# Kernel tuning notes

Measured on AMD Instinct MI355X. Metric: run time of the kernel, lower is better.

The kernel has to match this reference:

```python
import jax, jax.numpy as jnp
import numpy as np

D_MODEL = 64
N_HEADS = 4
D_K = 16
D_FF = 512
N_LAYERS = 6
SRC_V = 83
DEG_V = 21
DIST_V = 200
B, L = 256, 128


def _positional_encoding(length, d_model):
    pos = np.arange(length, dtype=np.float32)[:, None]
    div = np.exp(np.arange(0, d_model, 2, dtype=np.float32) * (-np.log(10000.0) / d_model))
    pe = np.zeros((length, d_model), dtype=np.float32)
    pe[:, 0::2] = np.sin(pos * div)
    pe[:, 1::2] = np.cos(pos * div)
    return jnp.asarray(pe)


def _layernorm(x, eps=1e-5):
    mu = jnp.mean(x, axis=-1, keepdims=True)
    var = jnp.mean((x - mu) ** 2, axis=-1, keepdims=True)
    return (x - mu) / jnp.sqrt(var + eps)


def setup_inputs() -> dict:
    key = jax.random.key(0)
    ks = jax.random.split(key, 12)
    s = 0.02
    enc_inputs = jax.random.randint(ks[0], (B, L), 0, SRC_V)
    degree_s = jax.random.randint(ks[1], (B, L), 0, DEG_V)
    MD = jax.random.randint(ks[2], (B, L, L), 0, DIST_V)
    src_emb = (jax.random.normal(ks[3], (SRC_V, D_MODEL)) * s).at[0].set(0.0)   # padding_idx=0
    deg_emb = (jax.random.normal(ks[4], (DEG_V, D_MODEL)) * s).at[20].set(0.0)  # padding_idx=20
    md_emb = (jax.random.normal(ks[5], (DIST_V, N_HEADS)) * s).at[0].set(0.0)   # padding_idx=0
    Wq = jax.random.normal(ks[6], (N_LAYERS, D_MODEL, N_HEADS * D_K)) * s
    Wk = jax.random.normal(ks[7], (N_LAYERS, D_MODEL, N_HEADS * D_K)) * s
    Wv = jax.random.normal(ks[8], (N_LAYERS, D_MODEL, N_HEADS * D_K)) * s
    Wo = jax.random.normal(ks[9], (N_LAYERS, N_HEADS * D_K, D_MODEL)) * s
    W1 = jax.random.normal(ks[10], (N_LAYERS, D_MODEL, D_FF)) * s
    W2 = jax.random.normal(ks[11], (N_LAYERS, D_FF, D_MODEL)) * s
    return dict(enc_inputs=enc_inputs, degree_s=degree_s, MD=MD,
                src_emb=src_emb, deg_emb=deg_emb, md_emb=md_emb,
                Wq=Wq, Wk=Wk, Wv=Wv, Wo=Wo, W1=W1, W2=W2)


def reference(enc_inputs, degree_s, MD, src_emb, deg_emb, md_emb, Wq, Wk, Wv, Wo, W1, W2):
    b, l = enc_inputs.shape
    x = src_emb[enc_inputs] + deg_emb[degree_s] + _positional_encoding(l, D_MODEL)[None]
    # pad mask: key token == 0 -> masked; broadcast [B,1,1,L] over heads & queries
    pad_mask = (enc_inputs == 0)[:, None, None, :]
    # distance bias: [B,L,L,H] -> [B,H,L,L]
    bias = jnp.transpose(md_emb[MD], (0, 3, 1, 2))
    scale = 1.0 / np.sqrt(D_K).astype(np.float32)
    for i in range(N_LAYERS):
        q = (x @ Wq[i]).reshape(b, l, N_HEADS, D_K).transpose(0, 2, 1, 3)
        k = (x @ Wk[i]).reshape(b, l, N_HEADS, D_K).transpose(0, 2, 1, 3)
        v = (x @ Wv[i]).reshape(b, l, N_HEADS, D_K).transpose(0, 2, 1, 3)
        scores = jnp.einsum('bhqd,bhkd->bhqk', q, k) * scale + bias
        scores = jnp.where(pad_mask, -1e9, scores)
        attn = jax.nn.softmax(scores, axis=-1)
        ctx = jnp.einsum('bhqk,bhkd->bhqd', attn, v).transpose(0, 2, 1, 3).reshape(b, l, N_HEADS * D_K)
        x = _layernorm(ctx @ Wo[i] + x)
        x = _layernorm(jax.nn.relu(x @ W1[i]) @ W2[i] + x)
    return x
```

## Files before the change

kernel.cpp:

```cpp
#include <hip/hip_runtime.h>
#include <hip/hip_bf16.h>
#include <stdint.h>

#define DI __device__ __forceinline__

namespace {

constexpr int BB  = 256;
constexpr int LL  = 128;
constexpr int DM  = 64;
constexpr int DFF = 512;
constexpr int NL  = 6;
constexpr int TT  = BB * LL;

typedef __attribute__((ext_vector_type(8))) short bf16x8;
typedef __attribute__((ext_vector_type(4))) float f32x4;

DI float bf2f(uint16_t u) { union { uint32_t i; float f; } w; w.i = (uint32_t)u << 16; return w.f; }
DI uint16_t f2bf(float f) {
  union { float f; uint32_t i; } w; w.f = f;
  uint32_t r = (w.i + 0x7fffu + ((w.i >> 16) & 1u)) >> 16;
  return (uint16_t)r;
}
DI uint32_t pack2(float a, float b) { return (uint32_t)f2bf(a) | ((uint32_t)f2bf(b) << 16); }

DI bf16x8 fragld(const uint16_t* __restrict__ base, int ld, int lane) {
  return *(const bf16x8*)(base + (size_t)(lane & 15) * ld + (lane >> 4) * 8);
}
DI f32x4 MFMA(bf16x8 a, bf16x8 b, f32x4 c) {
  return __builtin_amdgcn_mfma_f32_16x16x32_bf16(a, b, c, 0, 0, 0);
}

__global__ void __launch_bounds__(256) k_embed(const int* __restrict__ enc, const int* __restrict__ deg,
    const float* __restrict__ semb, const float* __restrict__ demb,
    float* __restrict__ x, uint16_t* __restrict__ xb) {
  int idx = blockIdx.x * 256 + threadIdx.x;
  int t = idx >> 6, d = idx & 63;
  int l = t & (LL - 1);
  float e = (float)(d & ~1) * -0.14391156831212787f;
  float ang = (float)l * __expf(e);
  float pe = (d & 1) ? __cosf(ang) : __sinf(ang);
  float v = semb[enc[t] * DM + d] + demb[deg[t] * DM + d] + pe;
  x[idx] = v;
  xb[idx] = f2bf(v);
}

__global__ void __launch_bounds__(256) k_trans(const float* __restrict__ w, uint16_t* __restrict__ wt,
    int K, int O, int dstStride, int colOff) {
  int idx = blockIdx.x * 256 + threadIdx.x;
  int KO = K * O;
  int mat = idx / KO;
  int rem = idx - mat * KO;
  int c = rem / K;
  int k = rem - c * K;
  wt[(size_t)mat * dstStride + (size_t)(colOff + c) * K + k] = f2bf(w[((size_t)mat * K + k) * O + c]);
}

__global__ void __launch_bounds__(256) k_bias2(const int* __restrict__ MD, const float* __restrict__ memb,
    const int* __restrict__ enc, uint16_t* __restrict__ biasT) {
  int o = blockIdx.x * 256 + threadIdx.x;
  int b  = o >> 14;
  int r  = (o >> 7) & (LL - 1);
  int kk = o & (LL - 1);
  bool mask = (enc[b * LL + kk] == 0);
  int md = MD[o];
  float4 m = *(const float4*)(memb + md * 4);
  float mv[4] = {m.x, m.y, m.z, m.w};
#pragma unroll
  for (int h = 0; h < 4; ++h) {
    uint16_t v = mask ? (uint16_t)0xce6eu : f2bf(mv[h]);
    biasT[(((size_t)(b * 4 + h) * LL) + r) * LL + kk] = v;
  }
}

DI void ln_write(float (&v)[4][4], float (&xfh)[4][4], uint16_t* __restrict__ xls,
                 int r0, int g, int c) {
  float sum[4], sq[4];
#pragma unroll
  for (int j = 0; j < 4; ++j) sum[j] = (v[j][0] + v[j][1]) + (v[j][2] + v[j][3]);
#pragma unroll
  for (int off = 1; off < 16; off <<= 1)
#pragma unroll
    for (int j = 0; j < 4; ++j) sum[j] += __shfl_xor(sum[j], off, 64);
#pragma unroll
  for (int j = 0; j < 4; ++j) {
    float mu = sum[j] * 0.015625f;
#pragma unroll
    for (int ct = 0; ct < 4; ++ct) v[j][ct] -= mu;
    sq[j] = (v[j][0] * v[j][0] + v[j][1] * v[j][1]) + (v[j][2] * v[j][2] + v[j][3] * v[j][3]);
  }
#pragma unroll
  for (int off = 1; off < 16; off <<= 1)
#pragma unroll
    for (int j = 0; j < 4; ++j) sq[j] += __shfl_xor(sq[j], off, 64);
#pragma unroll
  for (int j = 0; j < 4; ++j) {
    float rstd = rsqrtf(sq[j] * 0.015625f + 1e-5f);
#pragma unroll
    for (int ct = 0; ct < 4; ++ct) {
      float r = v[j][ct] * rstd;
      xfh[ct][j] = r;
      xls[(r0 + g * 4 + j) * 72 + ct * 16 + c] = f2bf(r);
    }
  }
}

__global__ void __launch_bounds__(512, 1) k_mega(
    const float* __restrict__ x0, const uint16_t* __restrict__ xb0,
    const uint16_t* __restrict__ biasT,
    const uint16_t* __restrict__ wtqkv, const uint16_t* __restrict__ wto,
    const uint16_t* __restrict__ wt1, const uint16_t* __restrict__ wt2,
    float* __restrict__ out) {
  __shared__ __align__(16) char LDSB[119808];
  int tid = threadIdx.x;
  int w8 = tid >> 6, lane = tid & 63;
  int g = lane >> 4, c = lane & 15;
  int h = w8 & 3, half = w8 >> 2;
  int b = blockIdx.x;

  uint16_t* xls  = (uint16_t*)(LDSB);
  uint16_t* klsA = (uint16_t*)(LDSB + 18432);
  uint16_t* klsh = (uint16_t*)(LDSB + 18432 + h * 10240);
  uint16_t* vtlh = (uint16_t*)(LDSB + 59392 + h * 4352);
  uint16_t* qsc  = (uint16_t*)(LDSB + 76800 + w8 * 1280);
  char*     ptl  = LDSB + 87040 + w8 * 4096;
  uint16_t* ctxl = (uint16_t*)(LDSB + 18432);
  uint16_t* hidl = (uint16_t*)(LDSB + 36864 + w8 * 8448);

  float xf[4][4];
  const float* xrow = x0 + ((size_t)b * LL + w8 * 16) * DM;
#pragma unroll
  for (int ct = 0; ct < 4; ++ct)
#pragma unroll
    for (int j = 0; j < 4; ++j)
      xf[ct][j] = xrow[(g * 4 + j) * DM + ct * 16 + c];
  const uint16_t* xbrow = xb0 + (size_t)b * LL * DM;
#pragma unroll
  for (int m = 0; m < 2; ++m) {
    int u = tid * 2 + m;
    int r = u >> 3, col = (u & 7) * 8;
    *(bf16x8*)(xls + r * 72 + col) = *(const bf16x8*)(xbrow + r * DM + col);
  }
  __syncthreads();

  for (int li = 0; li < NL; ++li) {
#pragma unroll
    for (int m = 0; m < 2; ++m) {
      int idx = tid * 2 + m;
      int head = idx >> 8, r = (idx >> 1) & 127, s = idx & 1;
      *(uint4*)(klsA + head * 5120 + r * 40 + 16 + s * 8) = uint4{0, 0, 0, 0};
    }
    if (lane < 32) {
      int r = lane >> 1, s = lane & 1;
      *(uint4*)(qsc + r * 40 + 16 + s * 8) = uint4{0, 0, 0, 0};
    }

    const uint16_t* Wl = wtqkv + (size_t)li * 192 * 64;
    bf16x8 bq0 = fragld(Wl + (h * 16) * 64, 64, lane);
    bf16x8 bq1 = fragld(Wl + (h * 16) * 64 + 32, 64, lane);
    bf16x8 bk0 = fragld(Wl + (64 + h * 16) * 64, 64, lane);
    bf16x8 bk1 = fragld(Wl + (64 + h * 16) * 64 + 32, 64, lane);
    bf16x8 bv0 = fragld(Wl + (128 + h * 16) * 64, 64, lane);
    bf16x8 bv1 = fragld(Wl + (128 + h * 16) * 64 + 32, 64, lane);
    uint2 qreg[4];
#pragma unroll
    for (int rt = 0; rt < 4; ++rt) {
      int r0 = half * 64 + rt * 16;
      bf16x8 a0 = fragld(xls + r0 * 72, 72, lane);
      bf16x8 a1 = fragld(xls + r0 * 72 + 32, 72, lane);
      f32x4 aq = {0,0,0,0}, ak = {0,0,0,0}, av = {0,0,0,0};
      aq = MFMA(a0, bq0, aq); aq = MFMA(a1, bq1, aq);
      ak = MFMA(a0, bk0, ak); ak = MFMA(a1, bk1, ak);
      av = MFMA(a0, bv0, av); av = MFMA(a1, bv1, av);
#pragma unroll
      for (int j = 0; j < 4; ++j)
        klsh[(r0 + g * 4 + j) * 40 + c] = f2bf(ak[j]);
      uint2 pk; pk.x = pack2(av[0], av[1]); pk.y = pack2(av[2], av[3]);
      *(uint2*)(vtlh + c * 136 + r0 + g * 4) = pk;
      qreg[rt].x = pack2(aq[0], aq[1]); qreg[rt].y = pack2(aq[2], aq[3]);
    }
    __syncthreads();

    bf16x8 kf[8], vf[4];
#pragma unroll
    for (int ct = 0; ct < 8; ++ct) kf[ct] = fragld(klsh + ct * 16 * 40, 40, lane);
#pragma unroll
    for (int kc = 0; kc < 4; ++kc) vf[kc] = fragld(vtlh + kc * 32, 136, lane);
    const uint16_t* bb = biasT + ((size_t)b * 4 + h) * (LL * LL);
    uint2 creg[4];
#pragma unroll 2
    for (int rt = 0; rt < 4; ++rt) {
      qsc[(g * 4 + 0) * 40 + c] = (uint16_t)(qreg[rt].x & 0xffff);
      qsc[(g * 4 + 1) * 40 + c] = (uint16_t)(qreg[rt].x >> 16);
      qsc[(g * 4 + 2) * 40 + c] = (uint16_t)(qreg[rt].y & 0xffff);
      qsc[(g * 4 + 3) * 40 + c] = (uint16_t)(qreg[rt].y >> 16);
      bf16x8 qf = fragld(qsc, 40, lane);
      f32x4 s[8];
#pragma unroll
      for (int ct = 0; ct < 8; ++ct) s[ct] = MFMA(qf, kf[ct], (f32x4){0.f, 0.f, 0.f, 0.f});
      {
        int rl = lane >> 2, seg = lane & 3;
        const uint16_t* gsrc = bb + (half * 64 + rt * 16 + rl) * LL + seg * 32;
#pragma unroll
        for (int m = 0; m < 4; ++m)
          *(bf16x8*)(ptl + rl * 256 + ((seg * 64 + m * 16) ^ ((rl & 7) << 4))) =
              *(const bf16x8*)(gsrc + m * 8);
      }
      float rs[4] = {0.f, 0.f, 0.f, 0.f};
#pragma unroll
      for (int ct = 0; ct < 8; ++ct) {
        int kk = ct * 16 + c;
#pragma unroll
        for (int j = 0; j < 4; ++j) {
          int row = g * 4 + j;
          char* addr = ptl + row * 256 + ((kk * 2) ^ ((row & 7) << 4));
          float bias = bf2f(*(uint16_t*)addr);
          float p = __expf(fmaf(s[ct][j], 0.25f, bias));
          rs[j] += p;
          *(uint16_t*)addr = f2bf(p);
        }
      }
#pragma unroll
      for (int off = 1; off < 16; off <<= 1)
#pragma unroll
        for (int j = 0; j < 4; ++j) rs[j] += __shfl_xor(rs[j], off, 64);
      f32x4 o = {0.f, 0.f, 0.f, 0.f};
#pragma unroll
      for (int kc = 0; kc < 4; ++kc) {
        bf16x8 af = *(const bf16x8*)(ptl + c * 256 + ((kc * 64 + g * 16) ^ ((c & 7) << 4)));
        o = MFMA(af, vf[kc], o);
      }
      creg[rt].x = pack2(o[0] / rs[0], o[1] / rs[1]);
      creg[rt].y = pack2(o[2] / rs[2], o[3] / rs[3]);
    }
    __syncthreads();

#pragma unroll
    for (int rt = 0; rt < 4; ++rt) {
      int r0 = half * 64 + rt * 16;
      ctxl[(r0 + g * 4 + 0) * 72 + h * 16 + c] = (uint16_t)(creg[rt].x & 0xffff);
      ctxl[(r0 + g * 4 + 1) * 72 + h * 16 + c] = (uint16_t)(creg[rt].x >> 16);
      ctxl[(r0 + g * 4 + 2) * 72 + h * 16 + c] = (uint16_t)(creg[rt].y & 0xffff);
      ctxl[(r0 + g * 4 + 3) * 72 + h * 16 + c] = (uint16_t)(creg[rt].y >> 16);
    }
    __syncthreads();

    int r0 = w8 * 16;
    {
      const uint16_t* Wol = wto + (size_t)li * 64 * 64;
      bf16x8 a0 = fragld(ctxl + r0 * 72, 72, lane);
      bf16x8 a1 = fragld(ctxl + r0 * 72 + 32, 72, lane);
      float v[4][4];
#pragma unroll
      for (int ct = 0; ct < 4; ++ct) {
        f32x4 acc = {0,0,0,0};
        acc = MFMA(a0, fragld(Wol + ct * 16 * 64, 64, lane), acc);
        acc = MFMA(a1, fragld(Wol + ct * 16 * 64 + 32, 64, lane), acc);
#pragma unroll
        for (int j = 0; j < 4; ++j) v[j][ct] = acc[j] + xf[ct][j];
      }
      ln_write(v, xf, xls, r0, g, c);
    }

    {
      const uint16_t* W1l = wt1 + (size_t)li * 512 * 64;
      const uint16_t* W2l = wt2 + (size_t)li * 64 * 512;
      bf16x8 a0 = fragld(xls + r0 * 72, 72, lane);
      bf16x8 a1 = fragld(xls + r0 * 72 + 32, 72, lane);
      f32x4 acc2[4] = {{0,0,0,0},{0,0,0,0},{0,0,0,0},{0,0,0,0}};
#pragma unroll
      for (int ffh = 0; ffh < 2; ++ffh) {
#pragma unroll 4
        for (int ct2 = 0; ct2 < 16; ++ct2) {
          int ctg = ffh * 16 + ct2;
          f32x4 acc = {0,0,0,0};
          acc = MFMA(a0, fragld(W1l + ctg * 16 * 64, 64, lane), acc);
          acc = MFMA(a1, fragld(W1l + ctg * 16 * 64 + 32, 64, lane), acc);
#pragma unroll
          for (int j = 0; j < 4; ++j)
            hidl[(g * 4 + j) * 264 + ct2 * 16 + c] = f2bf(fmaxf(acc[j], 0.f));
        }
#pragma unroll 4
        for (int kc2 = 0; kc2 < 8; ++kc2) {
          bf16x8 a = fragld(hidl + kc2 * 32, 264, lane);
#pragma unroll
          for (int ct = 0; ct < 4; ++ct)
            acc2[ct] = MFMA(a, fragld(W2l + ct * 16 * 512 + ffh * 256 + kc2 * 32, 512, lane), acc2[ct]);
        }
      }
      float v[4][4];
#pragma unroll
      for (int ct = 0; ct < 4; ++ct)
#pragma unroll
        for (int j = 0; j < 4; ++j) v[j][ct] = acc2[ct][j] + xf[ct][j];
      ln_write(v, xf, xls, r0, g, c);
    }
    __syncthreads();
  }

  float* orow = out + ((size_t)b * LL + w8 * 16) * DM;
#pragma unroll
  for (int ct = 0; ct < 4; ++ct)
#pragma unroll
    for (int j = 0; j < 4; ++j)
      orow[(g * 4 + j) * DM + ct * 16 + c] = xf[ct][j];
}

}

extern "C" void kernel_launch(void* const* d_in, const int* in_sizes, int n_in,
                              void* d_out, int out_size, void* d_ws, size_t ws_size,
                              hipStream_t stream) {
  const int* enc = (const int*)d_in[0];
  const int* deg = (const int*)d_in[1];
  const int* MD  = (const int*)d_in[2];
  const float* semb = (const float*)d_in[3];
  const float* demb = (const float*)d_in[4];
  const float* memb = (const float*)d_in[5];
  const float* Wq = (const float*)d_in[6];
  const float* Wk = (const float*)d_in[7];
  const float* Wv = (const float*)d_in[8];
  const float* Wo = (const float*)d_in[9];
  const float* W1 = (const float*)d_in[10];
  const float* W2 = (const float*)d_in[11];

  char* p = (char*)d_ws;
  float*    x    = (float*)p;     p += (size_t)TT * DM * 4;
  uint16_t* xb   = (uint16_t*)p;  p += (size_t)TT * DM * 2;
  uint16_t* biasT = (uint16_t*)p; p += (size_t)BB * 4 * LL * LL * 2;
  uint16_t* wtqkv = (uint16_t*)p; p += (size_t)NL * 192 * 64 * 2;
  uint16_t* wto   = (uint16_t*)p; p += (size_t)NL * 64 * 64 * 2;
  uint16_t* wt1   = (uint16_t*)p; p += (size_t)NL * 512 * 64 * 2;
  uint16_t* wt2   = (uint16_t*)p; p += (size_t)NL * 64 * 512 * 2;
  (void)ws_size; (void)in_sizes; (void)n_in; (void)out_size;

  k_embed<<<TT * DM / 256, 256, 0, stream>>>(enc, deg, semb, demb, x, xb);
  k_trans<<<NL * 64 * 64 / 256, 256, 0, stream>>>(Wq, wtqkv, 64, 64, 192 * 64, 0);
  k_trans<<<NL * 64 * 64 / 256, 256, 0, stream>>>(Wk, wtqkv, 64, 64, 192 * 64, 64);
  k_trans<<<NL * 64 * 64 / 256, 256, 0, stream>>>(Wv, wtqkv, 64, 64, 192 * 64, 128);
  k_trans<<<NL * 64 * 64 / 256, 256, 0, stream>>>(Wo, wto, 64, 64, 64 * 64, 0);
  k_trans<<<NL * 64 * 512 / 256, 256, 0, stream>>>(W1, wt1, 64, 512, 512 * 64, 0);
  k_trans<<<NL * 512 * 64 / 256, 256, 0, stream>>>(W2, wt2, 512, 64, 64 * 512, 0);
  k_bias2<<<BB * LL * LL / 256, 256, 0, stream>>>(MD, memb, enc, biasT);

  k_mega<<<BB, 512, 0, stream>>>(x, xb, biasT, wtqkv, wto, wt1, wt2, (float*)d_out);
}
```

Baseline: 306.8 us.

## Double block to 1024 threads, splitting rows and FFN across wave pairs

The fused encoder kernel now runs 16 waves per block instead of 8. Each wave handles half as many attention rows, and the output-projection, FFN and layernorm work is split across pairs of waves by column half. Partial FFN sums and layernorm statistics are exchanged through LDS with extra barriers. The bias tile is now read straight from global memory instead of being staged through LDS first. The aim is more latency hiding from the extra waves, at the cost of more synchronisation, a one-pass variance, and scattered global bias loads.

```diff
diff --git a/kernel.cpp b/kernel.cpp
--- a/kernel.cpp
+++ b/kernel.cpp
@@ -73,86 +73,52 @@
   }
 }
 
-DI void ln_write(float (&v)[4][4], float (&xfh)[4][4], uint16_t* __restrict__ xls,
-                 int r0, int g, int c) {
-  float sum[4], sq[4];
-#pragma unroll
-  for (int j = 0; j < 4; ++j) sum[j] = (v[j][0] + v[j][1]) + (v[j][2] + v[j][3]);
-#pragma unroll
-  for (int off = 1; off < 16; off <<= 1)
-#pragma unroll
-    for (int j = 0; j < 4; ++j) sum[j] += __shfl_xor(sum[j], off, 64);
-#pragma unroll
-  for (int j = 0; j < 4; ++j) {
-    float mu = sum[j] * 0.015625f;
-#pragma unroll
-    for (int ct = 0; ct < 4; ++ct) v[j][ct] -= mu;
-    sq[j] = (v[j][0] * v[j][0] + v[j][1] * v[j][1]) + (v[j][2] * v[j][2] + v[j][3] * v[j][3]);
-  }
-#pragma unroll
-  for (int off = 1; off < 16; off <<= 1)
-#pragma unroll
-    for (int j = 0; j < 4; ++j) sq[j] += __shfl_xor(sq[j], off, 64);
-#pragma unroll
-  for (int j = 0; j < 4; ++j) {
-    float rstd = rsqrtf(sq[j] * 0.015625f + 1e-5f);
-#pragma unroll
-    for (int ct = 0; ct < 4; ++ct) {
-      float r = v[j][ct] * rstd;
-      xfh[ct][j] = r;
-      xls[(r0 + g * 4 + j) * 72 + ct * 16 + c] = f2bf(r);
-    }
-  }
-}
-
-__global__ void __launch_bounds__(512, 1) k_mega(
+constexpr int LDS_TOTAL = 144384;
+
+__global__ void __launch_bounds__(1024, 4) k_mega(
     const float* __restrict__ x0, const uint16_t* __restrict__ xb0,
     const uint16_t* __restrict__ biasT,
     const uint16_t* __restrict__ wtqkv, const uint16_t* __restrict__ wto,
     const uint16_t* __restrict__ wt1, const uint16_t* __restrict__ wt2,
     float* __restrict__ out) {
-  __shared__ __align__(16) char LDSB[119808];
+  __shared__ __align__(16) char LDSB[LDS_TOTAL];
   int tid = threadIdx.x;
-  int w8 = tid >> 6, lane = tid & 63;
+  int w16 = tid >> 6, lane = tid & 63;
   int g = lane >> 4, c = lane & 15;
-  int h = w8 & 3, half = w8 >> 2;
+  int h  = w16 & 3, q4 = w16 >> 2;
+  int rt8 = w16 >> 1, ch = w16 & 1;
   int b = blockIdx.x;
 
   uint16_t* xls  = (uint16_t*)(LDSB);
   uint16_t* klsA = (uint16_t*)(LDSB + 18432);
   uint16_t* klsh = (uint16_t*)(LDSB + 18432 + h * 10240);
   uint16_t* vtlh = (uint16_t*)(LDSB + 59392 + h * 4352);
-  uint16_t* qsc  = (uint16_t*)(LDSB + 76800 + w8 * 1280);
-  char*     ptl  = LDSB + 87040 + w8 * 4096;
+  char*     ptlb = LDSB + 76800 + w16 * 4096;
   uint16_t* ctxl = (uint16_t*)(LDSB + 18432);
-  uint16_t* hidl = (uint16_t*)(LDSB + 36864 + w8 * 8448);
-
-  float xf[4][4];
-  const float* xrow = x0 + ((size_t)b * LL + w8 * 16) * DM;
-#pragma unroll
-  for (int ct = 0; ct < 4; ++ct)
+  uint16_t* hidl = (uint16_t*)(LDSB + 36864 + w16 * 4352);
+  char*     xchb = LDSB + 106496 + rt8 * 4096;
+  char*     lnb  = LDSB + 142336;
+
+  int r0 = rt8 * 16;
+
+  float xf[2][4];
+  const float* xrow = x0 + ((size_t)b * LL + r0) * DM + ch * 32;
+#pragma unroll
+  for (int ct2 = 0; ct2 < 2; ++ct2)
 #pragma unroll
     for (int j = 0; j < 4; ++j)
-      xf[ct][j] = xrow[(g * 4 + j) * DM + ct * 16 + c];
-  const uint16_t* xbrow = xb0 + (size_t)b * LL * DM;
-#pragma unroll
-  for (int m = 0; m < 2; ++m) {
-    int u = tid * 2 + m;
-    int r = u >> 3, col = (u & 7) * 8;
+      xf[ct2][j] = xrow[(g * 4 + j) * DM + ct2 * 16 + c];
+  {
+    const uint16_t* xbrow = xb0 + (size_t)b * LL * DM;
+    int r = tid >> 3, col = (tid & 7) * 8;
     *(bf16x8*)(xls + r * 72 + col) = *(const bf16x8*)(xbrow + r * DM + col);
   }
   __syncthreads();
 
   for (int li = 0; li < NL; ++li) {
-#pragma unroll
-    for (int m = 0; m < 2; ++m) {
-      int idx = tid * 2 + m;
-      int head = idx >> 8, r = (idx >> 1) & 127, s = idx & 1;
-      *(uint4*)(klsA + head * 5120 + r * 40 + 16 + s * 8) = uint4{0, 0, 0, 0};
-    }
-    if (lane < 32) {
-      int r = lane >> 1, s = lane & 1;
-      *(uint4*)(qsc + r * 40 + 16 + s * 8) = uint4{0, 0, 0, 0};
+    {
+      int head = tid >> 8, r = (tid >> 1) & 127, s = tid & 1;
+      *(uint4*)((char*)klsA + head * 10240 + r * 80 + 32 + s * 16) = uint4{0, 0, 0, 0};
     }
 
     const uint16_t* Wl = wtqkv + (size_t)li * 192 * 64;
@@ -162,21 +128,21 @@
     bf16x8 bk1 = fragld(Wl + (64 + h * 16) * 64 + 32, 64, lane);
     bf16x8 bv0 = fragld(Wl + (128 + h * 16) * 64, 64, lane);
     bf16x8 bv1 = fragld(Wl + (128 + h * 16) * 64 + 32, 64, lane);
-    uint2 qreg[4];
-#pragma unroll
-    for (int rt = 0; rt < 4; ++rt) {
-      int r0 = half * 64 + rt * 16;
-      bf16x8 a0 = fragld(xls + r0 * 72, 72, lane);
-      bf16x8 a1 = fragld(xls + r0 * 72 + 32, 72, lane);
+    uint2 qreg[2];
+#pragma unroll
+    for (int rt = 0; rt < 2; ++rt) {
+      int rr = q4 * 32 + rt * 16;
+      bf16x8 a0 = fragld(xls + rr * 72, 72, lane);
+      bf16x8 a1 = fragld(xls + rr * 72 + 32, 72, lane);
       f32x4 aq = {0,0,0,0}, ak = {0,0,0,0}, av = {0,0,0,0};
       aq = MFMA(a0, bq0, aq); aq = MFMA(a1, bq1, aq);
       ak = MFMA(a0, bk0, ak); ak = MFMA(a1, bk1, ak);
       av = MFMA(a0, bv0, av); av = MFMA(a1, bv1, av);
 #pragma unroll
       for (int j = 0; j < 4; ++j)
-        klsh[(r0 + g * 4 + j) * 40 + c] = f2bf(ak[j]);
+        klsh[(rr + g * 4 + j) * 40 + c] = f2bf(ak[j]);
       uint2 pk; pk.x = pack2(av[0], av[1]); pk.y = pack2(av[2], av[3]);
-      *(uint2*)(vtlh + c * 136 + r0 + g * 4) = pk;
+      *(uint2*)(vtlh + c * 136 + rr + g * 4) = pk;
       qreg[rt].x = pack2(aq[0], aq[1]); qreg[rt].y = pack2(aq[2], aq[3]);
     }
     __syncthreads();
@@ -187,9 +153,11 @@
 #pragma unroll
     for (int kc = 0; kc < 4; ++kc) vf[kc] = fragld(vtlh + kc * 32, 136, lane);
     const uint16_t* bb = biasT + ((size_t)b * 4 + h) * (LL * LL);
-    uint2 creg[4];
-#pragma unroll 2
-    for (int rt = 0; rt < 4; ++rt) {
+    uint2 creg[2];
+#pragma unroll
+    for (int rt = 0; rt < 2; ++rt) {
+      *(uint2*)(ptlb + (lane >> 2) * 80 + 32 + (lane & 3) * 8) = uint2{0, 0};
+      uint16_t* qsc = (uint16_t*)ptlb;
       qsc[(g * 4 + 0) * 40 + c] = (uint16_t)(qreg[rt].x & 0xffff);
       qsc[(g * 4 + 1) * 40 + c] = (uint16_t)(qreg[rt].x >> 16);
       qsc[(g * 4 + 2) * 40 + c] = (uint16_t)(qreg[rt].y & 0xffff);
@@ -198,26 +166,18 @@
       f32x4 s[8];
 #pragma unroll
       for (int ct = 0; ct < 8; ++ct) s[ct] = MFMA(qf, kf[ct], (f32x4){0.f, 0.f, 0.f, 0.f});
-      {
-        int rl = lane >> 2, seg = lane & 3;
-        const uint16_t* gsrc = bb + (half * 64 + rt * 16 + rl) * LL + seg * 32;
-#pragma unroll
-        for (int m = 0; m < 4; ++m)
-          *(bf16x8*)(ptl + rl * 256 + ((seg * 64 + m * 16) ^ ((rl & 7) << 4))) =
-              *(const bf16x8*)(gsrc + m * 8);
-      }
+      int rbase = q4 * 32 + rt * 16 + g * 4;
       float rs[4] = {0.f, 0.f, 0.f, 0.f};
 #pragma unroll
       for (int ct = 0; ct < 8; ++ct) {
         int kk = ct * 16 + c;
 #pragma unroll
         for (int j = 0; j < 4; ++j) {
-          int row = g * 4 + j;
-          char* addr = ptl + row * 256 + ((kk * 2) ^ ((row & 7) << 4));
-          float bias = bf2f(*(uint16_t*)addr);
+          float bias = bf2f(bb[(size_t)(rbase + j) * LL + kk]);
           float p = __expf(fmaf(s[ct][j], 0.25f, bias));
           rs[j] += p;
-          *(uint16_t*)addr = f2bf(p);
+          int row = g * 4 + j;
+          *(uint16_t*)(ptlb + row * 256 + ((kk * 2) ^ ((row & 7) << 4))) = f2bf(p);
         }
       }
 #pragma unroll
@@ -227,7 +187,7 @@
       f32x4 o = {0.f, 0.f, 0.f, 0.f};
 #pragma unroll
       for (int kc = 0; kc < 4; ++kc) {
-        bf16x8 af = *(const bf16x8*)(ptl + c * 256 + ((kc * 64 + g * 16) ^ ((c & 7) << 4)));
+        bf16x8 af = *(const bf16x8*)(ptlb + c * 256 + ((kc * 64 + g * 16) ^ ((c & 7) << 4)));
         o = MFMA(af, vf[kc], o);
       }
       creg[rt].x = pack2(o[0] / rs[0], o[1] / rs[1]);
@@ -236,31 +196,65 @@
     __syncthreads();
 
 #pragma unroll
-    for (int rt = 0; rt < 4; ++rt) {
-      int r0 = half * 64 + rt * 16;
-      ctxl[(r0 + g * 4 + 0) * 72 + h * 16 + c] = (uint16_t)(creg[rt].x & 0xffff);
-      ctxl[(r0 + g * 4 + 1) * 72 + h * 16 + c] = (uint16_t)(creg[rt].x >> 16);
-      ctxl[(r0 + g * 4 + 2) * 72 + h * 16 + c] = (uint16_t)(creg[rt].y & 0xffff);
-      ctxl[(r0 + g * 4 + 3) * 72 + h * 16 + c] = (uint16_t)(creg[rt].y >> 16);
-    }
-    __syncthreads();
-
-    int r0 = w8 * 16;
+    for (int rt = 0; rt < 2; ++rt) {
+      int rr = q4 * 32 + rt * 16;
+      ctxl[(rr + g * 4 + 0) * 72 + h * 16 + c] = (uint16_t)(creg[rt].x & 0xffff);
+      ctxl[(rr + g * 4 + 1) * 72 + h * 16 + c] = (uint16_t)(creg[rt].x >> 16);
+      ctxl[(rr + g * 4 + 2) * 72 + h * 16 + c] = (uint16_t)(creg[rt].y & 0xffff);
+      ctxl[(rr + g * 4 + 3) * 72 + h * 16 + c] = (uint16_t)(creg[rt].y >> 16);
+    }
+    __syncthreads();
+
     {
       const uint16_t* Wol = wto + (size_t)li * 64 * 64;
       bf16x8 a0 = fragld(ctxl + r0 * 72, 72, lane);
       bf16x8 a1 = fragld(ctxl + r0 * 72 + 32, 72, lane);
-      float v[4][4];
-#pragma unroll
-      for (int ct = 0; ct < 4; ++ct) {
+      float v[4][2];
+#pragma unroll
+      for (int ct2 = 0; ct2 < 2; ++ct2) {
+        int ct = ch * 2 + ct2;
         f32x4 acc = {0,0,0,0};
         acc = MFMA(a0, fragld(Wol + ct * 16 * 64, 64, lane), acc);
         acc = MFMA(a1, fragld(Wol + ct * 16 * 64 + 32, 64, lane), acc);
 #pragma unroll
-        for (int j = 0; j < 4; ++j) v[j][ct] = acc[j] + xf[ct][j];
-      }
-      ln_write(v, xf, xls, r0, g, c);
-    }
+        for (int j = 0; j < 4; ++j) v[j][ct2] = acc[j] + xf[ct2][j];
+      }
+      float ps[4], pq[4];
+#pragma unroll
+      for (int j = 0; j < 4; ++j) {
+        ps[j] = v[j][0] + v[j][1];
+        pq[j] = v[j][0] * v[j][0] + v[j][1] * v[j][1];
+      }
+#pragma unroll
+      for (int off = 1; off < 16; off <<= 1)
+#pragma unroll
+        for (int j = 0; j < 4; ++j) {
+          ps[j] += __shfl_xor(ps[j], off, 64);
+          pq[j] += __shfl_xor(pq[j], off, 64);
+        }
+      if (c == 0) {
+#pragma unroll
+        for (int j = 0; j < 4; ++j)
+          *(float2*)(lnb + (r0 + g * 4 + j) * 16 + ch * 8) = float2{ps[j], pq[j]};
+      }
+      __syncthreads();
+#pragma unroll
+      for (int j = 0; j < 4; ++j) {
+        int row = r0 + g * 4 + j;
+        float2 m0 = *(const float2*)(lnb + row * 16);
+        float2 m1 = *(const float2*)(lnb + row * 16 + 8);
+        float mu = (m0.x + m1.x) * 0.015625f;
+        float var = (m0.y + m1.y) * 0.015625f - mu * mu;
+        float rstd = rsqrtf(var + 1e-5f);
+#pragma unroll
+        for (int ct2 = 0; ct2 < 2; ++ct2) {
+          float r = (v[j][ct2] - mu) * rstd;
+          xf[ct2][j] = r;
+          xls[row * 72 + ch * 32 + ct2 * 16 + c] = f2bf(r);
+        }
+      }
+    }
+    __syncthreads();
 
     {
       const uint16_t* W1l = wt1 + (size_t)li * 512 * 64;
@@ -269,41 +263,87 @@
       bf16x8 a1 = fragld(xls + r0 * 72 + 32, 72, lane);
       f32x4 acc2[4] = {{0,0,0,0},{0,0,0,0},{0,0,0,0},{0,0,0,0}};
 #pragma unroll
-      for (int ffh = 0; ffh < 2; ++ffh) {
+      for (int fh = 0; fh < 2; ++fh) {
 #pragma unroll 4
-        for (int ct2 = 0; ct2 < 16; ++ct2) {
-          int ctg = ffh * 16 + ct2;
+        for (int ct2 = 0; ct2 < 8; ++ct2) {
+          int ctg = ch * 16 + fh * 8 + ct2;
           f32x4 acc = {0,0,0,0};
           acc = MFMA(a0, fragld(W1l + ctg * 16 * 64, 64, lane), acc);
           acc = MFMA(a1, fragld(W1l + ctg * 16 * 64 + 32, 64, lane), acc);
 #pragma unroll
           for (int j = 0; j < 4; ++j)
-            hidl[(g * 4 + j) * 264 + ct2 * 16 + c] = f2bf(fmaxf(acc[j], 0.f));
+            hidl[(g * 4 + j) * 136 + ct2 * 16 + c] = f2bf(fmaxf(acc[j], 0.f));
         }
 #pragma unroll 4
-        for (int kc2 = 0; kc2 < 8; ++kc2) {
-          bf16x8 a = fragld(hidl + kc2 * 32, 264, lane);
+        for (int kc = 0; kc < 4; ++kc) {
+          bf16x8 a = fragld(hidl + kc * 32, 136, lane);
+          int kg = ch * 256 + fh * 128 + kc * 32;
 #pragma unroll
           for (int ct = 0; ct < 4; ++ct)
-            acc2[ct] = MFMA(a, fragld(W2l + ct * 16 * 512 + ffh * 256 + kc2 * 32, 512, lane), acc2[ct]);
-        }
-      }
-      float v[4][4];
-#pragma unroll
-      for (int ct = 0; ct < 4; ++ct)
-#pragma unroll
-        for (int j = 0; j < 4; ++j) v[j][ct] = acc2[ct][j] + xf[ct][j];
-      ln_write(v, xf, xls, r0, g, c);
+            acc2[ct] = MFMA(a, fragld(W2l + ct * 16 * 512 + kg, 512, lane), acc2[ct]);
+        }
+      }
+      int och = ch ^ 1;
+#pragma unroll
+      for (int ct2 = 0; ct2 < 2; ++ct2) {
+        f32x4 t = acc2[och * 2 + ct2];
+#pragma unroll
+        for (int j = 0; j < 4; ++j)
+          *(float*)(xchb + och * 2048 + (g * 4 + j) * 128 + (ct2 * 16 + c) * 4) = t[j];
+      }
+      __syncthreads();
+      float v[4][2];
+#pragma unroll
+      for (int ct2 = 0; ct2 < 2; ++ct2)
+#pragma unroll
+        for (int j = 0; j < 4; ++j) {
+          float part = *(const float*)(xchb + ch * 2048 + (g * 4 + j) * 128 + (ct2 * 16 + c) * 4);
+          v[j][ct2] = acc2[ch * 2 + ct2][j] + part + xf[ct2][j];
+        }
+      float ps[4], pq[4];
+#pragma unroll
+      for (int j = 0; j < 4; ++j) {
+        ps[j] = v[j][0] + v[j][1];
+        pq[j] = v[j][0] * v[j][0] + v[j][1] * v[j][1];
+      }
+#pragma unroll
+      for (int off = 1; off < 16; off <<= 1)
+#pragma unroll
+        for (int j = 0; j < 4; ++j) {
+          ps[j] += __shfl_xor(ps[j], off, 64);
+          pq[j] += __shfl_xor(pq[j], off, 64);
+        }
+      if (c == 0) {
+#pragma unroll
+        for (int j = 0; j < 4; ++j)
+          *(float2*)(lnb + (r0 + g * 4 + j) * 16 + ch * 8) = float2{ps[j], pq[j]};
+      }
+      __syncthreads();
+#pragma unroll
+      for (int j = 0; j < 4; ++j) {
+        int row = r0 + g * 4 + j;
+        float2 m0 = *(const float2*)(lnb + row * 16);
+        float2 m1 = *(const float2*)(lnb + row * 16 + 8);
+        float mu = (m0.x + m1.x) * 0.015625f;
+        float var = (m0.y + m1.y) * 0.015625f - mu * mu;
+        float rstd = rsqrtf(var + 1e-5f);
+#pragma unroll
+        for (int ct2 = 0; ct2 < 2; ++ct2) {
+          float r = (v[j][ct2] - mu) * rstd;
+          xf[ct2][j] = r;
+          xls[row * 72 + ch * 32 + ct2 * 16 + c] = f2bf(r);
+        }
+      }
     }
     __syncthreads();
   }
 
-  float* orow = out + ((size_t)b * LL + w8 * 16) * DM;
-#pragma unroll
-  for (int ct = 0; ct < 4; ++ct)
+  float* orow = out + ((size_t)b * LL + r0) * DM + ch * 32;
+#pragma unroll
+  for (int ct2 = 0; ct2 < 2; ++ct2)
 #pragma unroll
     for (int j = 0; j < 4; ++j)
-      orow[(g * 4 + j) * DM + ct * 16 + c] = xf[ct][j];
+      orow[(g * 4 + j) * DM + ct2 * 16 + c] = xf[ct2][j];
 }
 
 }
@@ -343,5 +383,5 @@
   k_trans<<<NL * 512 * 64 / 256, 256, 0, stream>>>(W2, wt2, 512, 64, 64 * 512, 0);
   k_bias2<<<BB * LL * LL / 256, 256, 0, stream>>>(MD, memb, enc, biasT);
 
-  k_mega<<<BB, 512, 0, stream>>>(x, xb, biasT, wtqkv, wto, wt1, wt2, (float*)d_out);
-}
+  k_mega<<<BB, 1024, 0, stream>>>(x, xb, biasT, wtqkv, wto, wt1, wt2, (float*)d_out);
+}
```

Measured after the change: 499.2 us. +62.7%, slower.

## Prefetch bias tiles into registers and give ctx its own LDS region

Applied to the files above, without the earlier changes.

The attention row-tile loop becomes a templated, fully unrolled sequence. Each step prefetches the next 16-row bias tile from global memory into registers (double buffered) while it computes the current tile, and the first tile is loaded before the barrier. The context buffer moves to a separate LDS region, so ctx can be written straight from the attention phase and one __syncthreads per layer goes away. V fragments are now reloaded from LDS inside each step rather than held in registers. The costs are more LDS use (138KB) and higher register pressure.

```diff
diff --git a/kernel.cpp b/kernel.cpp
--- a/kernel.cpp
+++ b/kernel.cpp
@@ -105,13 +105,73 @@
   }
 }
 
+constexpr int LDS_TOTAL = 138240;
+
+template<int RT>
+DI void attn_rt(bf16x8 (&cur)[4], bf16x8 (&nxt)[4],
+                const uint16_t* __restrict__ bb, int hrow0,
+                char* ptlb, uint16_t* qsc, const bf16x8 (&kf)[8],
+                const uint16_t* vtlh, const uint2 (&qreg)[4], uint2 (&creg)[4],
+                int lane, int g, int c) {
+  int rl = lane >> 2, seg = lane & 3;
+  int swz = (rl & 7) << 4;
+  *(bf16x8*)(ptlb + rl * 256 + ((seg * 64 +  0) ^ swz)) = cur[0];
+  *(bf16x8*)(ptlb + rl * 256 + ((seg * 64 + 16) ^ swz)) = cur[1];
+  *(bf16x8*)(ptlb + rl * 256 + ((seg * 64 + 32) ^ swz)) = cur[2];
+  *(bf16x8*)(ptlb + rl * 256 + ((seg * 64 + 48) ^ swz)) = cur[3];
+  if (RT < 3) {
+    const uint16_t* gs = bb + (size_t)(hrow0 + (RT + 1) * 16 + rl) * LL + seg * 32;
+    nxt[0] = *(const bf16x8*)(gs);
+    nxt[1] = *(const bf16x8*)(gs + 8);
+    nxt[2] = *(const bf16x8*)(gs + 16);
+    nxt[3] = *(const bf16x8*)(gs + 24);
+  }
+  qsc[(g * 4 + 0) * 40 + c] = (uint16_t)(qreg[RT].x & 0xffff);
+  qsc[(g * 4 + 1) * 40 + c] = (uint16_t)(qreg[RT].x >> 16);
+  qsc[(g * 4 + 2) * 40 + c] = (uint16_t)(qreg[RT].y & 0xffff);
+  qsc[(g * 4 + 3) * 40 + c] = (uint16_t)(qreg[RT].y >> 16);
+  bf16x8 qf = fragld(qsc, 40, lane);
+  f32x4 s[8];
+#pragma unroll
+  for (int ct = 0; ct < 8; ++ct) s[ct] = MFMA(qf, kf[ct], (f32x4){0.f, 0.f, 0.f, 0.f});
+  float rs[4] = {0.f, 0.f, 0.f, 0.f};
+#pragma unroll
+  for (int ct = 0; ct < 8; ++ct) {
+    int kk = ct * 16 + c;
+#pragma unroll
+    for (int j = 0; j < 4; ++j) {
+      int row = g * 4 + j;
+      char* addr = ptlb + row * 256 + ((kk * 2) ^ ((row & 7) << 4));
+      float bias = bf2f(*(uint16_t*)addr);
+      float p = __expf(fmaf(s[ct][j], 0.25f, bias));
+      rs[j] += p;
+      *(uint16_t*)addr = f2bf(p);
+    }
+  }
+#pragma unroll
+  for (int off = 1; off < 16; off <<= 1)
+#pragma unroll
+    for (int j = 0; j < 4; ++j) rs[j] += __shfl_xor(rs[j], off, 64);
+  bf16x8 vf[4];
+#pragma unroll
+  for (int kc = 0; kc < 4; ++kc) vf[kc] = fragld(vtlh + kc * 32, 136, lane);
+  f32x4 o = {0.f, 0.f, 0.f, 0.f};
+#pragma unroll
+  for (int kc = 0; kc < 4; ++kc) {
+    bf16x8 af = *(const bf16x8*)(ptlb + c * 256 + ((kc * 64 + g * 16) ^ ((c & 7) << 4)));
+    o = MFMA(af, vf[kc], o);
+  }
+  creg[RT].x = pack2(o[0] / rs[0], o[1] / rs[1]);
+  creg[RT].y = pack2(o[2] / rs[2], o[3] / rs[3]);
+}
+
 __global__ void __launch_bounds__(512, 1) k_mega(
     const float* __restrict__ x0, const uint16_t* __restrict__ xb0,
     const uint16_t* __restrict__ biasT,
     const uint16_t* __restrict__ wtqkv, const uint16_t* __restrict__ wto,
     const uint16_t* __restrict__ wt1, const uint16_t* __restrict__ wt2,
     float* __restrict__ out) {
-  __shared__ __align__(16) char LDSB[119808];
+  __shared__ __align__(16) char LDSB[LDS_TOTAL];
   int tid = threadIdx.x;
   int w8 = tid >> 6, lane = tid & 63;
   int g = lane >> 4, c = lane & 15;
@@ -119,40 +179,46 @@
   int b = blockIdx.x;
 
   uint16_t* xls  = (uint16_t*)(LDSB);
-  uint16_t* klsA = (uint16_t*)(LDSB + 18432);
+  char*     klsA = LDSB + 18432;
   uint16_t* klsh = (uint16_t*)(LDSB + 18432 + h * 10240);
   uint16_t* vtlh = (uint16_t*)(LDSB + 59392 + h * 4352);
   uint16_t* qsc  = (uint16_t*)(LDSB + 76800 + w8 * 1280);
-  char*     ptl  = LDSB + 87040 + w8 * 4096;
-  uint16_t* ctxl = (uint16_t*)(LDSB + 18432);
-  uint16_t* hidl = (uint16_t*)(LDSB + 36864 + w8 * 8448);
+  char*     ptlb = LDSB + 87040 + w8 * 4096;
+  uint16_t* ctxl = (uint16_t*)(LDSB + 119808);
+  uint16_t* hidl = (uint16_t*)(LDSB + 18432 + w8 * 8448);
+
+  int r0 = w8 * 16;
+  int hrow0 = half * 64;
 
   float xf[4][4];
-  const float* xrow = x0 + ((size_t)b * LL + w8 * 16) * DM;
+  const float* xrow = x0 + ((size_t)b * LL + r0) * DM;
 #pragma unroll
   for (int ct = 0; ct < 4; ++ct)
 #pragma unroll
     for (int j = 0; j < 4; ++j)
       xf[ct][j] = xrow[(g * 4 + j) * DM + ct * 16 + c];
-  const uint16_t* xbrow = xb0 + (size_t)b * LL * DM;
-#pragma unroll
-  for (int m = 0; m < 2; ++m) {
-    int u = tid * 2 + m;
-    int r = u >> 3, col = (u & 7) * 8;
-    *(bf16x8*)(xls + r * 72 + col) = *(const bf16x8*)(xbrow + r * DM + col);
-  }
+  {
+    const uint16_t* xbrow = xb0 + (size_t)b * LL * DM;
+#pragma unroll
+    for (int m = 0; m < 2; ++m) {
+      int u = tid * 2 + m;
+      int r = u >> 3, col = (u & 7) * 8;
+      *(bf16x8*)(xls + r * 72 + col) = *(const bf16x8*)(xbrow + r * DM + col);
+    }
+  }
+  const uint16_t* bb = biasT + ((size_t)b * 4 + h) * (LL * LL);
   __syncthreads();
 
   for (int li = 0; li < NL; ++li) {
 #pragma unroll
     for (int m = 0; m < 2; ++m) {
       int idx = tid * 2 + m;
-      int head = idx >> 8, r = (idx >> 1) & 127, s = idx & 1;
-      *(uint4*)(klsA + head * 5120 + r * 40 + 16 + s * 8) = uint4{0, 0, 0, 0};
+      int head = idx >> 8, r = (idx >> 1) & 127, s2 = idx & 1;
+      *(uint4*)(klsA + head * 10240 + r * 80 + 32 + s2 * 16) = uint4{0, 0, 0, 0};
     }
     if (lane < 32) {
-      int r = lane >> 1, s = lane & 1;
-      *(uint4*)(qsc + r * 40 + 16 + s * 8) = uint4{0, 0, 0, 0};
+      int r = lane >> 1, s2 = lane & 1;
+      *(uint4*)((char*)qsc + r * 80 + 32 + s2 * 16) = uint4{0, 0, 0, 0};
     }
 
     const uint16_t* Wl = wtqkv + (size_t)li * 192 * 64;
@@ -165,87 +231,50 @@
     uint2 qreg[4];
 #pragma unroll
     for (int rt = 0; rt < 4; ++rt) {
-      int r0 = half * 64 + rt * 16;
-      bf16x8 a0 = fragld(xls + r0 * 72, 72, lane);
-      bf16x8 a1 = fragld(xls + r0 * 72 + 32, 72, lane);
+      int rr = hrow0 + rt * 16;
+      bf16x8 a0 = fragld(xls + rr * 72, 72, lane);
+      bf16x8 a1 = fragld(xls + rr * 72 + 32, 72, lane);
       f32x4 aq = {0,0,0,0}, ak = {0,0,0,0}, av = {0,0,0,0};
       aq = MFMA(a0, bq0, aq); aq = MFMA(a1, bq1, aq);
       ak = MFMA(a0, bk0, ak); ak = MFMA(a1, bk1, ak);
       av = MFMA(a0, bv0, av); av = MFMA(a1, bv1, av);
 #pragma unroll
       for (int j = 0; j < 4; ++j)
-        klsh[(r0 + g * 4 + j) * 40 + c] = f2bf(ak[j]);
+        klsh[(rr + g * 4 + j) * 40 + c] = f2bf(ak[j]);
       uint2 pk; pk.x = pack2(av[0], av[1]); pk.y = pack2(av[2], av[3]);
-      *(uint2*)(vtlh + c * 136 + r0 + g * 4) = pk;
+      *(uint2*)(vtlh + c * 136 + rr + g * 4) = pk;
       qreg[rt].x = pack2(aq[0], aq[1]); qreg[rt].y = pack2(aq[2], aq[3]);
     }
+    bf16x8 bregA[4], bregB[4];
+    {
+      int rl = lane >> 2, seg = lane & 3;
+      const uint16_t* gs = bb + (size_t)(hrow0 + rl) * LL + seg * 32;
+      bregA[0] = *(const bf16x8*)(gs);
+      bregA[1] = *(const bf16x8*)(gs + 8);
+      bregA[2] = *(const bf16x8*)(gs + 16);
+      bregA[3] = *(const bf16x8*)(gs + 24);
+    }
     __syncthreads();
 
-    bf16x8 kf[8], vf[4];
+    bf16x8 kf[8];
 #pragma unroll
     for (int ct = 0; ct < 8; ++ct) kf[ct] = fragld(klsh + ct * 16 * 40, 40, lane);
-#pragma unroll
-    for (int kc = 0; kc < 4; ++kc) vf[kc] = fragld(vtlh + kc * 32, 136, lane);
-    const uint16_t* bb = biasT + ((size_t)b * 4 + h) * (LL * LL);
     uint2 creg[4];
-#pragma unroll 2
+    attn_rt<0>(bregA, bregB, bb, hrow0, ptlb, qsc, kf, vtlh, qreg, creg, lane, g, c);
+    attn_rt<1>(bregB, bregA, bb, hrow0, ptlb, qsc, kf, vtlh, qreg, creg, lane, g, c);
+    attn_rt<2>(bregA, bregB, bb, hrow0, ptlb, qsc, kf, vtlh, qreg, creg, lane, g, c);
+    attn_rt<3>(bregB, bregA, bb, hrow0, ptlb, qsc, kf, vtlh, qreg, creg, lane, g, c);
+
+#pragma unroll
     for (int rt = 0; rt < 4; ++rt) {
-      qsc[(g * 4 + 0) * 40 + c] = (uint16_t)(qreg[rt].x & 0xffff);
-      qsc[(g * 4 + 1) * 40 + c] = (uint16_t)(qreg[rt].x >> 16);
-      qsc[(g * 4 + 2) * 40 + c] = (uint16_t)(qreg[rt].y & 0xffff);
-      qsc[(g * 4 + 3) * 40 + c] = (uint16_t)(qreg[rt].y >> 16);
-      bf16x8 qf = fragld(qsc, 40, lane);
-      f32x4 s[8];
-#pragma unroll
-      for (int ct = 0; ct < 8; ++ct) s[ct] = MFMA(qf, kf[ct], (f32x4){0.f, 0.f, 0.f, 0.f});
-      {
-        int rl = lane >> 2, seg = lane & 3;
-        const uint16_t* gsrc = bb + (half * 64 + rt * 16 + rl) * LL + seg * 32;
-#pragma unroll
-        for (int m = 0; m < 4; ++m)
-          *(bf16x8*)(ptl + rl * 256 + ((seg * 64 + m * 16) ^ ((rl & 7) << 4))) =
-              *(const bf16x8*)(gsrc + m * 8);
-      }
-      float rs[4] = {0.f, 0.f, 0.f, 0.f};
-#pragma unroll
-      for (int ct = 0; ct < 8; ++ct) {
-        int kk = ct * 16 + c;
-#pragma unroll
-        for (int j = 0; j < 4; ++j) {
-          int row = g * 4 + j;
-          char* addr = ptl + row * 256 + ((kk * 2) ^ ((row & 7) << 4));
-          float bias = bf2f(*(uint16_t*)addr);
-          float p = __expf(fmaf(s[ct][j], 0.25f, bias));
-          rs[j] += p;
-          *(uint16_t*)addr = f2bf(p);
-        }
-      }
-#pragma unroll
-      for (int off = 1; off < 16; off <<= 1)
-#pragma unroll
-        for (int j = 0; j < 4; ++j) rs[j] += __shfl_xor(rs[j], off, 64);
-      f32x4 o = {0.f, 0.f, 0.f, 0.f};
-#pragma unroll
-      for (int kc = 0; kc < 4; ++kc) {
-        bf16x8 af = *(const bf16x8*)(ptl + c * 256 + ((kc * 64 + g * 16) ^ ((c & 7) << 4)));
-        o = MFMA(af, vf[kc], o);
-      }
-      creg[rt].x = pack2(o[0] / rs[0], o[1] / rs[1]);
-      creg[rt].y = pack2(o[2] / rs[2], o[3] / rs[3]);
+      int rr = hrow0 + rt * 16;
+      ctxl[(rr + g * 4 + 0) * 72 + h * 16 + c] = (uint16_t)(creg[rt].x & 0xffff);
+      ctxl[(rr + g * 4 + 1) * 72 + h * 16 + c] = (uint16_t)(creg[rt].x >> 16);
+      ctxl[(rr + g * 4 + 2) * 72 + h * 16 + c] = (uint16_t)(creg[rt].y & 0xffff);
+      ctxl[(rr + g * 4 + 3) * 72 + h * 16 + c] = (uint16_t)(creg[rt].y >> 16);
     }
     __syncthreads();
 
-#pragma unroll
-    for (int rt = 0; rt < 4; ++rt) {
-      int r0 = half * 64 + rt * 16;
-      ctxl[(r0 + g * 4 + 0) * 72 + h * 16 + c] = (uint16_t)(creg[rt].x & 0xffff);
-      ctxl[(r0 + g * 4 + 1) * 72 + h * 16 + c] = (uint16_t)(creg[rt].x >> 16);
-      ctxl[(r0 + g * 4 + 2) * 72 + h * 16 + c] = (uint16_t)(creg[rt].y & 0xffff);
-      ctxl[(r0 + g * 4 + 3) * 72 + h * 16 + c] = (uint16_t)(creg[rt].y >> 16);
-    }
-    __syncthreads();
-
-    int r0 = w8 * 16;
     {
       const uint16_t* Wol = wto + (size_t)li * 64 * 64;
       bf16x8 a0 = fragld(ctxl + r0 * 72, 72, lane);
@@ -269,10 +298,10 @@
       bf16x8 a1 = fragld(xls + r0 * 72 + 32, 72, lane);
       f32x4 acc2[4] = {{0,0,0,0},{0,0,0,0},{0,0,0,0},{0,0,0,0}};
 #pragma unroll
-      for (int ffh = 0; ffh < 2; ++ffh) {
+      for (int fh = 0; fh < 2; ++fh) {
 #pragma unroll 4
         for (int ct2 = 0; ct2 < 16; ++ct2) {
-          int ctg = ffh * 16 + ct2;
+          int ctg = fh * 16 + ct2;
           f32x4 acc = {0,0,0,0};
           acc = MFMA(a0, fragld(W1l + ctg * 16 * 64, 64, lane), acc);
           acc = MFMA(a1, fragld(W1l + ctg * 16 * 64 + 32, 64, lane), acc);
@@ -283,9 +312,10 @@
 #pragma unroll 4
         for (int kc2 = 0; kc2 < 8; ++kc2) {
           bf16x8 a = fragld(hidl + kc2 * 32, 264, lane);
+          int kg = fh * 256 + kc2 * 32;
 #pragma unroll
           for (int ct = 0; ct < 4; ++ct)
-            acc2[ct] = MFMA(a, fragld(W2l + ct * 16 * 512 + ffh * 256 + kc2 * 32, 512, lane), acc2[ct]);
+            acc2[ct] = MFMA(a, fragld(W2l + ct * 16 * 512 + kg, 512, lane), acc2[ct]);
         }
       }
       float v[4][4];
@@ -298,7 +328,7 @@
     __syncthreads();
   }
 
-  float* orow = out + ((size_t)b * LL + w8 * 16) * DM;
+  float* orow = out + ((size_t)b * LL + r0) * DM;
 #pragma unroll
   for (int ct = 0; ct < 4; ++ct)
 #pragma unroll
```

Result: no change. 303.5 us (median of 2 runs) (-1.1%).
